# Performance work log

Measured on AMD Instinct MI355X. Metric: run time of the kernel, lower is better.

## Reference

```python
import jax, jax.numpy as jnp
import numpy as np

K = 5          # kernel_size
PAD = (K - 1) // 2  # fixed_padding with dilation=1, stride=1 -> 'same'


def setup_inputs() -> dict:
    key = jax.random.key(0)
    kx, kw = jax.random.split(key)
    x = jax.random.normal(kx, (4, 8, 512, 512), dtype=jnp.float32)
    # nn.Parameter initialized to zeros in the original; use small random values
    # so the op is non-trivial (math is identical for any weight values).
    weight = jax.random.normal(kw, (8, 8, K, K), dtype=jnp.float32) * 0.05
    return {"x": x, "weight": weight}


def reference(x, weight):
    """Morphological dilation2d with hard max (soft_max=False).

    out[n,o,h,w] = max_{c,dy,dx} ( x_pad[n,c,h+dy,w+dx] + weight[o,c,dy,dx] )
    Faithful to: pad zeros -> unfold -> weight + x -> max over dim C*k*k.
    Computed as a fused sliding-window max-plus reduction (no (N,C,k,k,H,W)
    unfold tensor is materialized; loop is over the fixed k*k kernel taps).
    """
    N, C, H, W = x.shape
    O = weight.shape[0]
    xp = jnp.pad(x, ((0, 0), (0, 0), (PAD, PAD), (PAD, PAD)))  # zero pad, as in F.pad
    out = jnp.full((N, O, H, W), -jnp.inf, dtype=x.dtype)
    for dy in range(K):
        for dx in range(K):
            patch = xp[:, :, dy:dy + H, dx:dx + W]           # (N,C,H,W)
            w_tap = weight[:, :, dy, dx]                      # (O,C)
            # (N,1,C,H,W) + (1,O,C,1,1) -> max over C -> (N,O,H,W)
            term = patch[:, None] + w_tap[None, :, :, None, None]
            out = jnp.maximum(out, jnp.max(term, axis=2))
    return out
```

## Files before the change

kernel.cpp:

```cpp
#include <hip/hip_runtime.h>
#include <math.h>
#include <stdint.h>

typedef _Float16 half2v __attribute__((ext_vector_type(2)));

#define KK 5
#define PADK 2
#define C_IN 8
#define O_OUT 8
#define HH 512
#define WW 512
#define TH 8
#define TW 64
#define LROWS (TH + 2 * PADK)
#define LPAIRS 36
#define NW (O_OUT * C_IN * KK * KK)

static __device__ __forceinline__ half2v bc_h2(uint32_t u) {
    return __builtin_bit_cast(half2v, u);
}
static __device__ __forceinline__ half2v emax(half2v a, half2v b) {
    return __builtin_elementwise_max(a, b);
}

__global__ void prep_weights_kernel(const float* __restrict__ w,
                                    uint32_t* __restrict__ wp) {
    int i = blockIdx.x * 256 + threadIdx.x;
    if (i < NW) {
        int dx = i % KK;
        int t  = i / KK;
        int dy = t % KK;  t /= KK;
        int c  = t % C_IN;
        int o  = t / C_IN;
        _Float16 h = (_Float16)w[i];
        uint16_t hb = __builtin_bit_cast(uint16_t, h);
        int j = ((c * KK + dy) * O_OUT + o) * KK + dx;
        wp[j] = ((uint32_t)hb << 16) | (uint32_t)hb;
    }
}

template <bool USE_WS>
__global__ __launch_bounds__(256, 8)
void dil_kernel(const float* __restrict__ x,
                const float* __restrict__ wf,
                const uint32_t* __restrict__ wp,
                float* __restrict__ out) {
    __shared__ uint32_t lds[C_IN][LROWS][LPAIRS];

    const int tid = threadIdx.x;
    const int w0 = blockIdx.x * TW;
    const int h0 = blockIdx.y * TH;
    const int n  = blockIdx.z;

    const float* xn = x + (size_t)n * (C_IN * HH * WW);
    for (int idx = tid; idx < C_IN * LROWS * LPAIRS; idx += 256) {
        int c   = idx / (LROWS * LPAIRS);
        int rem = idx - c * (LROWS * LPAIRS);
        int r   = rem / LPAIRS;
        int jp  = rem - r * LPAIRS;
        int gh = h0 - PADK + r;
        int gw = w0 - PADK + 2 * jp;
        float v0 = 0.f, v1 = 0.f;
        if ((unsigned)gh < (unsigned)HH) {
            const float* row = xn + ((size_t)c * HH + gh) * WW;
            if ((unsigned)gw < (unsigned)WW) v0 = row[gw];
            if ((unsigned)(gw + 1) < (unsigned)WW) v1 = row[gw + 1];
        }
        _Float16 a = (_Float16)v0, b = (_Float16)v1;
        uint32_t u = ((uint32_t)__builtin_bit_cast(uint16_t, b) << 16) |
                     (uint32_t)__builtin_bit_cast(uint16_t, a);
        (&lds[0][0][0])[idx] = u;
    }
    __syncthreads();

    const int tx = tid & 31;
    const int ty = tid >> 5;

    const uint32_t NINF = 0xFC00FC00u;
    half2v acc[O_OUT];
    #pragma unroll
    for (int o = 0; o < O_OUT; ++o) acc[o] = bc_h2(NINF);

    for (int c = 0; c < C_IN; ++c) {
        #pragma unroll
        for (int dy = 0; dy < KK; ++dy) {
            const uint32_t* lrow = &lds[c][ty + dy][tx];
            uint32_t u0 = lrow[0];
            uint32_t u1 = lrow[1];
            uint32_t u2 = lrow[2];
            uint32_t s0 = (u0 >> 16) | (u1 << 16);
            uint32_t s1 = (u1 >> 16) | (u2 << 16);
            half2v H0 = bc_h2(u0), H1 = bc_h2(u1), H2 = bc_h2(u2);
            half2v S0 = bc_h2(s0), S1 = bc_h2(s1);

            const int wbase = (c * KK + dy) * (O_OUT * KK);
            #pragma unroll
            for (int o = 0; o < O_OUT; ++o) {
                half2v W0, W1, W2, W3, W4;
                if (USE_WS) {
                    const int off = wbase + o * KK;
                    W0 = bc_h2(wp[off + 0]);
                    W1 = bc_h2(wp[off + 1]);
                    W2 = bc_h2(wp[off + 2]);
                    W3 = bc_h2(wp[off + 3]);
                    W4 = bc_h2(wp[off + 4]);
                } else {
                    const int off = ((o * C_IN + c) * KK + dy) * KK;
                    _Float16 h0w = (_Float16)wf[off + 0];
                    _Float16 h1w = (_Float16)wf[off + 1];
                    _Float16 h2w = (_Float16)wf[off + 2];
                    _Float16 h3w = (_Float16)wf[off + 3];
                    _Float16 h4w = (_Float16)wf[off + 4];
                    W0 = (half2v){h0w, h0w}; W1 = (half2v){h1w, h1w};
                    W2 = (half2v){h2w, h2w}; W3 = (half2v){h3w, h3w};
                    W4 = (half2v){h4w, h4w};
                }
                half2v t0 = H0 + W0, t1 = S0 + W1, t2 = H1 + W2,
                       t3 = S1 + W3, t4 = H2 + W4;
                half2v m01 = emax(t0, t1), m23 = emax(t2, t3);
                acc[o] = emax(acc[o], emax(emax(m01, m23), t4));
            }
        }
    }

    float* onp = out + (size_t)n * (O_OUT * HH * WW);
    const int h = h0 + ty;
    const int wcol = w0 + 2 * tx;
    #pragma unroll
    for (int o = 0; o < O_OUT; ++o) {
        float2 r;
        r.x = (float)acc[o].x;
        r.y = (float)acc[o].y;
        *(float2*)(&onp[((size_t)o * HH + h) * WW + wcol]) = r;
    }
}

extern "C" void kernel_launch(void* const* d_in, const int* in_sizes, int n_in,
                              void* d_out, int out_size, void* d_ws, size_t ws_size,
                              hipStream_t stream) {
    const float* x   = (const float*)d_in[0];
    const float* wgt = (const float*)d_in[1];
    float* out = (float*)d_out;

    dim3 grid(WW / TW, HH / TH, 4);
    dim3 block(256);

    if (ws_size >= (size_t)NW * 4) {
        uint32_t* wp = (uint32_t*)d_ws;
        prep_weights_kernel<<<(NW + 255) / 256, 256, 0, stream>>>(wgt, wp);
        dil_kernel<true><<<grid, block, 0, stream>>>(x, wgt, wp, out);
    } else {
        dil_kernel<false><<<grid, block, 0, stream>>>(x, wgt, nullptr, out);
    }
}
```

Baseline: 74.98 us.

## Widen tile to 128 columns with one wavefront per row and uniform weight loads

Each block now covers 128 columns with 512 threads, so every 64-wide wavefront owns one output row. The row index is made wave-uniform with readfirstlane, which lets the weight reads become scalar loads. The channel loop is rotated per wave to stagger LDS access, and all LDS reads for a channel are hoisted ahead of the compute. The halo overhead per tile drops, but the grid halves, and the larger block with launch bounds of 512 may raise register pressure or lower occupancy.

```diff
diff --git a/kernel.cpp b/kernel.cpp
--- a/kernel.cpp
+++ b/kernel.cpp
@@ -11,9 +11,9 @@
 #define HH 512
 #define WW 512
 #define TH 8
-#define TW 64
+#define TW 128
 #define LROWS (TH + 2 * PADK)
-#define LPAIRS 36
+#define LPAIRS 68
 #define NW (O_OUT * C_IN * KK * KK)
 
 static __device__ __forceinline__ half2v bc_h2(uint32_t u) {
@@ -40,7 +40,7 @@
 }
 
 template <bool USE_WS>
-__global__ __launch_bounds__(256, 8)
+__global__ __launch_bounds__(512, 8)
 void dil_kernel(const float* __restrict__ x,
                 const float* __restrict__ wf,
                 const uint32_t* __restrict__ wp,
@@ -53,7 +53,7 @@
     const int n  = blockIdx.z;
 
     const float* xn = x + (size_t)n * (C_IN * HH * WW);
-    for (int idx = tid; idx < C_IN * LROWS * LPAIRS; idx += 256) {
+    for (int idx = tid; idx < C_IN * LROWS * LPAIRS; idx += 512) {
         int c   = idx / (LROWS * LPAIRS);
         int rem = idx - c * (LROWS * LPAIRS);
         int r   = rem / LPAIRS;
@@ -73,37 +73,45 @@
     }
     __syncthreads();
 
-    const int tx = tid & 31;
-    const int ty = tid >> 5;
+    const int tx  = tid & 63;
+    const int wid = __builtin_amdgcn_readfirstlane(tid >> 6);
 
     const uint32_t NINF = 0xFC00FC00u;
     half2v acc[O_OUT];
     #pragma unroll
     for (int o = 0; o < O_OUT; ++o) acc[o] = bc_h2(NINF);
 
-    for (int c = 0; c < C_IN; ++c) {
+    for (int ci = 0; ci < C_IN; ++ci) {
+        const int c = (ci + wid) & 7;
+
+        uint32_t u[KK][3];
         #pragma unroll
         for (int dy = 0; dy < KK; ++dy) {
-            const uint32_t* lrow = &lds[c][ty + dy][tx];
-            uint32_t u0 = lrow[0];
-            uint32_t u1 = lrow[1];
-            uint32_t u2 = lrow[2];
+            const uint32_t* lrow = &lds[c][wid + dy][tx];
+            u[dy][0] = lrow[0];
+            u[dy][1] = lrow[1];
+            u[dy][2] = lrow[2];
+        }
+
+        const uint32_t* wc = wp + c * (KK * O_OUT * KK);
+        #pragma unroll
+        for (int dy = 0; dy < KK; ++dy) {
+            uint32_t u0 = u[dy][0], u1 = u[dy][1], u2 = u[dy][2];
             uint32_t s0 = (u0 >> 16) | (u1 << 16);
             uint32_t s1 = (u1 >> 16) | (u2 << 16);
             half2v H0 = bc_h2(u0), H1 = bc_h2(u1), H2 = bc_h2(u2);
             half2v S0 = bc_h2(s0), S1 = bc_h2(s1);
 
-            const int wbase = (c * KK + dy) * (O_OUT * KK);
             #pragma unroll
             for (int o = 0; o < O_OUT; ++o) {
                 half2v W0, W1, W2, W3, W4;
                 if (USE_WS) {
-                    const int off = wbase + o * KK;
-                    W0 = bc_h2(wp[off + 0]);
-                    W1 = bc_h2(wp[off + 1]);
-                    W2 = bc_h2(wp[off + 2]);
-                    W3 = bc_h2(wp[off + 3]);
-                    W4 = bc_h2(wp[off + 4]);
+                    const uint32_t* wd = wc + dy * (O_OUT * KK) + o * KK;
+                    W0 = bc_h2(wd[0]);
+                    W1 = bc_h2(wd[1]);
+                    W2 = bc_h2(wd[2]);
+                    W3 = bc_h2(wd[3]);
+                    W4 = bc_h2(wd[4]);
                 } else {
                     const int off = ((o * C_IN + c) * KK + dy) * KK;
                     _Float16 h0w = (_Float16)wf[off + 0];
@@ -124,7 +132,7 @@
     }
 
     float* onp = out + (size_t)n * (O_OUT * HH * WW);
-    const int h = h0 + ty;
+    const int h = h0 + wid;
     const int wcol = w0 + 2 * tx;
     #pragma unroll
     for (int o = 0; o < O_OUT; ++o) {
@@ -143,7 +151,7 @@
     float* out = (float*)d_out;
 
     dim3 grid(WW / TW, HH / TH, 4);
-    dim3 block(256);
+    dim3 block(512);
 
     if (ws_size >= (size_t)NW * 4) {
         uint32_t* wp = (uint32_t*)d_ws;
```

Result: no change. 74.83 us (-0.2%).
